# Performance work log

Measured on AMD Instinct MI355X. Metric: run time of the kernel, lower is better.

## Reference

```python
import jax, jax.numpy as jnp
import numpy as np

NUM_HEADS = 16


def setup_inputs() -> dict:
    key = jax.random.key(0)
    ks = jax.random.split(key, 7)
    B, Nq, Nkv = 8, 1024, 2048
    q_dim, kv_dim, hidden = 1024, 1152, 1024
    s = 0.02
    return {
        "vision_latents": jax.random.normal(ks[0], (B, Nkv, kv_dim), jnp.float32),
        "queries": jax.random.normal(ks[1], (B, Nq, q_dim), jnp.float32),
        "attention_mask": jnp.zeros((B, Nkv), dtype=bool),
        "Wq": jax.random.normal(ks[2], (hidden, q_dim), jnp.float32) * s,
        "Wk": jax.random.normal(ks[3], (hidden, kv_dim), jnp.float32) * s,
        "Wv": jax.random.normal(ks[4], (hidden, kv_dim), jnp.float32) * s,
        "Wo": jax.random.normal(ks[5], (hidden, hidden), jnp.float32) * s,
    }


def reference(vision_latents, queries, attention_mask, Wq, Wk, Wv, Wo):
    B, Nq, _ = queries.shape
    Nkv = vision_latents.shape[1]
    H = NUM_HEADS
    hidden = Wq.shape[0]
    D = hidden // H  # head_dim

    # projections (nn.Linear: x @ W.T), split heads -> [B, H, S, D]
    q = (queries @ Wq.T).reshape(B, Nq, H, D).transpose(0, 2, 1, 3)
    k = (vision_latents @ Wk.T).reshape(B, Nkv, H, D).transpose(0, 2, 1, 3)
    v = (vision_latents @ Wv.T).reshape(B, Nkv, H, D).transpose(0, 2, 1, 3)

    scale = 1.0 / np.sqrt(D).astype(np.float32)
    scores = jnp.einsum("bhqd,bhkd->bhqk", q, k) * scale  # [B,H,Nq,Nkv]
    scores = jnp.where(attention_mask[:, None, None, :], jnp.float32(-1e9), scores)
    probs = jax.nn.softmax(scores, axis=-1)
    attn = jnp.einsum("bhqk,bhkd->bhqd", probs, v)  # [B,H,Nq,D]
    attn = attn.transpose(0, 2, 1, 3).reshape(B, Nq, hidden)
    return attn @ Wo.T
```

## Files before the change

kernel.cpp:

```cpp
#include <hip/hip_runtime.h>
#include <stdint.h>

typedef __attribute__((ext_vector_type(8))) __bf16 bf16x8;
typedef __attribute__((ext_vector_type(4))) float f32x4;
typedef __attribute__((ext_vector_type(4))) unsigned short u16x4;
typedef __attribute__((ext_vector_type(4))) unsigned char u8x4;

#define DEV __device__ __forceinline__

DEV unsigned short f2bf(float f) {
  return __builtin_bit_cast(unsigned short, (__bf16)f);
}

DEV void gload16(const void* g, void* l) {
  __builtin_amdgcn_global_load_lds(
      (const __attribute__((address_space(1))) unsigned int*)g,
      (__attribute__((address_space(3))) unsigned int*)l, 16, 0, 0);
}

__global__ __launch_bounds__(256) void cvt_bf16_kernel(
    const float* __restrict__ in, unsigned short* __restrict__ out, int n4) {
  int i = blockIdx.x * blockDim.x + threadIdx.x;
  int stride = gridDim.x * blockDim.x;
  const f32x4* in4 = (const f32x4*)in;
  u16x4* out4 = (u16x4*)out;
  for (; i < n4; i += stride) {
    f32x4 v = in4[i];
    u16x4 o;
    o[0] = f2bf(v[0]); o[1] = f2bf(v[1]); o[2] = f2bf(v[2]); o[3] = f2bf(v[3]);
    out4[i] = o;
  }
}

template <int EPI>
__global__ __launch_bounds__(256, 2) void gemm_bt_kernel(
    const unsigned short* __restrict__ A, const unsigned short* __restrict__ W,
    void* __restrict__ Cout, int M, int N, int K, int logS) {
  __shared__ unsigned short sA[128 * 32];
  __shared__ unsigned short sB[128 * 32];
  const int t = threadIdx.x;
  const int w = t >> 6;
  const int lane = t & 63;
  const int lr = lane & 15;
  const int kg = lane >> 4;
  const int row0 = blockIdx.y * 128;
  const int col0 = blockIdx.x * 128;

  const unsigned short* srcA = A + (size_t)(row0 + (t >> 2)) * K + (t & 3) * 8;
  const unsigned short* srcB = W + (size_t)(col0 + (t >> 2)) * K + (t & 3) * 8;
  const size_t rowSkip = (size_t)64 * K;

  char* sAb = (char*)sA + w * 1024;
  char* sBb = (char*)sB + w * 1024;

  f32x4 acc[4][4];
#pragma unroll
  for (int i = 0; i < 4; i++)
#pragma unroll
    for (int j = 0; j < 4; j++) acc[i][j] = f32x4{0.f, 0.f, 0.f, 0.f};

  const int wr = (w >> 1) * 64;
  const int wc = (w & 1) * 64;

  for (int k0 = 0; k0 < K; k0 += 32) {
    __syncthreads();
    gload16(srcA, sAb);
    gload16(srcA + rowSkip, sAb + 4096);
    gload16(srcB, sBb);
    gload16(srcB + rowSkip, sBb + 4096);
    srcA += 32;
    srcB += 32;
    __syncthreads();

    bf16x8 af[4], bfr[4];
#pragma unroll
    for (int mi = 0; mi < 4; mi++)
      af[mi] = *(const bf16x8*)&sA[(wr + mi * 16 + lr) * 32 + kg * 8];
#pragma unroll
    for (int ni = 0; ni < 4; ni++)
      bfr[ni] = *(const bf16x8*)&sB[(wc + ni * 16 + lr) * 32 + kg * 8];
#pragma unroll
    for (int mi = 0; mi < 4; mi++)
#pragma unroll
      for (int ni = 0; ni < 4; ni++)
        acc[mi][ni] = __builtin_amdgcn_mfma_f32_16x16x32_bf16(
            af[mi], bfr[ni], acc[mi][ni], 0, 0, 0);
  }

  const int S1 = 1 << logS;
  if (EPI == 2) {
    float* O = (float*)Cout;
#pragma unroll
    for (int mi = 0; mi < 4; mi++) {
      int gm0 = row0 + wr + mi * 16 + kg * 4;
#pragma unroll
      for (int ni = 0; ni < 4; ni++) {
        int gn = col0 + wc + ni * 16 + lr;
#pragma unroll
        for (int j = 0; j < 4; j++)
          O[(size_t)(gm0 + j) * N + gn] = acc[mi][ni][j];
      }
    }
  } else if (EPI == 0) {
    unsigned short* O = (unsigned short*)Cout;
#pragma unroll
    for (int mi = 0; mi < 4; mi++) {
      int gm0 = row0 + wr + mi * 16 + kg * 4;
      int b = gm0 >> logS;
      int s = gm0 & (S1 - 1);
#pragma unroll
      for (int ni = 0; ni < 4; ni++) {
        int gn = col0 + wc + ni * 16 + lr;
        int h = gn >> 6, d = gn & 63;
        size_t base = (((size_t)(b * 16 + h) << logS) + s) * 64 + d;
#pragma unroll
        for (int j = 0; j < 4; j++)
          O[base + (size_t)j * 64] = f2bf(acc[mi][ni][j]);
      }
    }
  } else {
    unsigned short* O = (unsigned short*)Cout;
#pragma unroll
    for (int mi = 0; mi < 4; mi++) {
      int gm0 = row0 + wr + mi * 16 + kg * 4;
      int b = gm0 >> logS;
      int s = gm0 & (S1 - 1);
#pragma unroll
      for (int ni = 0; ni < 4; ni++) {
        int gn = col0 + wc + ni * 16 + lr;
        int h = gn >> 6, d = gn & 63;
        u16x4 pk;
#pragma unroll
        for (int j = 0; j < 4; j++) pk[j] = f2bf(acc[mi][ni][j]);
        *(u16x4*)&O[(((size_t)(b * 16 + h) * 64 + d) << logS) + s] = pk;
      }
    }
  }
}

__global__ __launch_bounds__(256, 4) void flash_kernel(
    const unsigned short* __restrict__ Qb, const unsigned short* __restrict__ Kb,
    const unsigned short* __restrict__ Vt, const unsigned char* __restrict__ mask,
    unsigned short* __restrict__ attn) {
  constexpr int NQ = 1024, NKV = 2048, H = 16;
  constexpr float K1 = 0.18033688011112042f;
  __shared__ unsigned short sK[64 * 64];
  __shared__ unsigned short sV[64 * 64];
  __shared__ unsigned short sP[4][32 * 72];

  const int t = threadIdx.x;
  const int w = t >> 6;
  const int lane = t & 63;
  const int c = lane & 15;
  const int g = lane >> 4;
  const int n = blockIdx.x;
  const int bh = n & 127;
  const int b = bh >> 4;
  const int q0 = (n >> 7) * 128 + w * 32;

  bf16x8 qfrag[2][2];
#pragma unroll
  for (int qf = 0; qf < 2; qf++)
#pragma unroll
    for (int kf = 0; kf < 2; kf++)
      qfrag[qf][kf] = *(const bf16x8*)&Qb[((size_t)bh * NQ + q0 + qf * 16 + c) * 64 +
                                          kf * 32 + g * 8];

  const int srow = t >> 3;
  const int sw = (t & 7) ^ (srow & 7);
  const unsigned short* srcK = Kb + ((size_t)bh * NKV + srow) * 64 + sw * 8;
  const unsigned short* srcV = Vt + ((size_t)bh * 64 + srow) * NKV + sw * 8;
  char* sKb = (char*)sK + w * 1024;
  char* sVb = (char*)sV + w * 1024;

  float lrun[2] = {0.f, 0.f};
  f32x4 acc_o[2][4];
#pragma unroll
  for (int i = 0; i < 2; i++)
#pragma unroll
    for (int j = 0; j < 4; j++) acc_o[i][j] = f32x4{0.f, 0.f, 0.f, 0.f};

  const unsigned char* mrow = mask + (size_t)b * NKV;

  for (int kv0 = 0; kv0 < NKV; kv0 += 64) {
    __syncthreads();
    gload16(srcK, sKb);
    gload16(srcK + 32 * 64, sKb + 4096);
    gload16(srcV, sVb);
    gload16(srcV + (size_t)32 * NKV, sVb + 4096);
    srcK += 64 * 64;
    srcV += 64;
    __syncthreads();

    f32x4 accs[4][2];
#pragma unroll
    for (int kvf = 0; kvf < 4; kvf++) {
      int row = kvf * 16 + c;
      const char* rb = (const char*)sK + row * 128;
      bf16x8 ka = *(const bf16x8*)(rb + ((g) ^ (row & 7)) * 16);
      bf16x8 kb = *(const bf16x8*)(rb + ((4 + g) ^ (row & 7)) * 16);
#pragma unroll
      for (int qf = 0; qf < 2; qf++) {
        f32x4 z = f32x4{0.f, 0.f, 0.f, 0.f};
        z = __builtin_amdgcn_mfma_f32_16x16x32_bf16(ka, qfrag[qf][0], z, 0, 0, 0);
        accs[kvf][qf] =
            __builtin_amdgcn_mfma_f32_16x16x32_bf16(kb, qfrag[qf][1], z, 0, 0, 0);
      }
    }

    float mb[4][4];
#pragma unroll
    for (int kvf = 0; kvf < 4; kvf++) {
      u8x4 mm = *(const u8x4*)&mrow[kv0 + kvf * 16 + g * 4];
#pragma unroll
      for (int j = 0; j < 4; j++) mb[kvf][j] = mm[j] ? -30000.0f : 0.0f;
    }

#pragma unroll
    for (int qf = 0; qf < 2; qf++) {
      float ssum = 0.f;
#pragma unroll
      for (int kvf = 0; kvf < 4; kvf++) {
        u16x4 pk;
#pragma unroll
        for (int j = 0; j < 4; j++) {
          float p = exp2f(accs[kvf][qf][j] * K1 + mb[kvf][j]);
          ssum += p;
          pk[j] = f2bf(p);
        }
        *(u16x4*)&sP[w][(qf * 16 + c) * 72 + kvf * 16 + g * 4] = pk;
      }
      ssum += __shfl_xor(ssum, 16);
      ssum += __shfl_xor(ssum, 32);
      lrun[qf] += ssum;
    }

#pragma unroll
    for (int kvs = 0; kvs < 2; kvs++) {
      bf16x8 pa[2];
#pragma unroll
      for (int mi = 0; mi < 2; mi++)
        pa[mi] = *(const bf16x8*)&sP[w][(mi * 16 + c) * 72 + kvs * 32 + g * 8];
#pragma unroll
      for (int nf = 0; nf < 4; nf++) {
        int row = nf * 16 + c;
        bf16x8 vb = *(const bf16x8*)((const char*)sV + row * 128 +
                                     ((kvs * 4 + g) ^ (row & 7)) * 16);
#pragma unroll
        for (int mi = 0; mi < 2; mi++)
          acc_o[mi][nf] = __builtin_amdgcn_mfma_f32_16x16x32_bf16(
              pa[mi], vb, acc_o[mi][nf], 0, 0, 0);
      }
    }
  }

  const int h = bh & 15;
#pragma unroll
  for (int mi = 0; mi < 2; mi++) {
    f32x4 rj;
#pragma unroll
    for (int j = 0; j < 4; j++) rj[j] = 1.0f / __shfl(lrun[mi], g * 4 + j);
    size_t qbase = (size_t)b * NQ + q0 + mi * 16 + g * 4;
#pragma unroll
    for (int j = 0; j < 4; j++) {
      size_t rowb = ((qbase + j) * H + h) * 64;
#pragma unroll
      for (int nf = 0; nf < 4; nf++)
        attn[rowb + nf * 16 + c] = f2bf(acc_o[mi][nf][j] * rj[j]);
    }
  }
}

extern "C" void kernel_launch(void* const* d_in, const int* in_sizes, int n_in,
                              void* d_out, int out_size, void* d_ws, size_t ws_size,
                              hipStream_t stream) {
  const float* vision = (const float*)d_in[0];
  const float* queries = (const float*)d_in[1];
  const unsigned char* mask = (const unsigned char*)d_in[2];
  const float* Wq = (const float*)d_in[3];
  const float* Wk = (const float*)d_in[4];
  const float* Wv = (const float*)d_in[5];
  const float* Wo = (const float*)d_in[6];

  constexpr int B = 8, NQ = 1024, NKV = 2048, HID = 1024, KVD = 1152;
  constexpr size_t nQin = (size_t)B * NQ * HID;
  constexpr size_t nVis = (size_t)B * NKV * KVD;
  constexpr size_t nWq = (size_t)HID * HID;
  constexpr size_t nWk = (size_t)HID * KVD;
  constexpr size_t nQb = (size_t)B * 16 * NQ * 64;
  constexpr size_t nKb = (size_t)B * 16 * NKV * 64;

  constexpr size_t need = (2 * (nWq + nWk) + nVis + nQb + 2 * nKb) * 2;
  if (ws_size < need) {
    hipMemsetAsync(d_out, 0, (size_t)out_size * sizeof(float), stream);
    return;
  }

  char* p = (char*)d_ws;
  unsigned short* wqb = (unsigned short*)p;  p += nWq * 2;
  unsigned short* wkb = (unsigned short*)p;  p += nWk * 2;
  unsigned short* wvb = (unsigned short*)p;  p += nWk * 2;
  unsigned short* wob = (unsigned short*)p;  p += nWq * 2;
  unsigned short* slotA = (unsigned short*)p; p += nVis * 2;
  unsigned short* Qb = (unsigned short*)p;   p += nQb * 2;
  unsigned short* Kbf = (unsigned short*)p;  p += nKb * 2;
  unsigned short* Vtb = (unsigned short*)p;

  unsigned short* qbf = slotA;
  unsigned short* vbf = slotA;
  unsigned short* attnb = slotA;

  auto cvt = [&](const float* in, unsigned short* out, size_t n) {
    int n4 = (int)(n / 4);
    int blocks = (n4 + 255) / 256;
    if (blocks > 2048) blocks = 2048;
    cvt_bf16_kernel<<<dim3(blocks), dim3(256), 0, stream>>>(in, out, n4);
  };
  cvt(Wq, wqb, nWq);
  cvt(Wk, wkb, nWk);
  cvt(Wv, wvb, nWk);
  cvt(Wo, wob, nWq);

  cvt(queries, qbf, nQin);
  gemm_bt_kernel<0><<<dim3(8, 64), dim3(256), 0, stream>>>(qbf, wqb, Qb, 8192, 1024, 1024, 10);

  cvt(vision, vbf, nVis);
  gemm_bt_kernel<0><<<dim3(8, 128), dim3(256), 0, stream>>>(vbf, wkb, Kbf, 16384, 1024, 1152, 11);
  gemm_bt_kernel<1><<<dim3(8, 128), dim3(256), 0, stream>>>(vbf, wvb, Vtb, 16384, 1024, 1152, 11);

  flash_kernel<<<dim3(1024), dim3(256), 0, stream>>>(Qb, Kbf, Vtb, mask, attnb);

  gemm_bt_kernel<2><<<dim3(8, 64), dim3(256), 0, stream>>>(attnb, wob, d_out, 8192, 1024, 1024, 10);
}
```

Baseline: 484.5 us.

## Fuse K/V projections into one GEMM and read K/V from global memory in flash

Merges the K and V projection GEMMs into a single launch with N=2048, which relies on Wk and Wv being contiguous in the workspace and on K and Vt being contiguous. The flash kernel drops its LDS staging of K/V and the block barriers, loading fragments straight from global memory and relying on cache hits. Blocks are remapped so neighbouring blocks share a head, the occupancy hint drops to 3, and raw v_exp/v_rcp instructions replace exp2f and division. The risk is exposed global-load latency and uncoalesced fragment loads where LDS staging used to hide them.

```diff
diff --git a/kernel.cpp b/kernel.cpp
--- a/kernel.cpp
+++ b/kernel.cpp
@@ -10,6 +10,17 @@
 
 DEV unsigned short f2bf(float f) {
   return __builtin_bit_cast(unsigned short, (__bf16)f);
+}
+
+DEV float fast_exp2(float x) {
+  float r;
+  asm("v_exp_f32 %0, %1" : "=v"(r) : "v"(x));
+  return r;
+}
+DEV float fast_rcp(float x) {
+  float r;
+  asm("v_rcp_f32 %0, %1" : "=v"(r) : "v"(x));
+  return r;
 }
 
 DEV void gload16(const void* g, void* l) {
@@ -120,32 +131,40 @@
     }
   } else {
     unsigned short* O = (unsigned short*)Cout;
+    constexpr size_t VOFF = (size_t)8 * 16 * 2048 * 64;
 #pragma unroll
     for (int mi = 0; mi < 4; mi++) {
       int gm0 = row0 + wr + mi * 16 + kg * 4;
-      int b = gm0 >> logS;
-      int s = gm0 & (S1 - 1);
+      int b = gm0 >> 11;
+      int s = gm0 & 2047;
 #pragma unroll
       for (int ni = 0; ni < 4; ni++) {
         int gn = col0 + wc + ni * 16 + lr;
-        int h = gn >> 6, d = gn & 63;
-        u16x4 pk;
-#pragma unroll
-        for (int j = 0; j < 4; j++) pk[j] = f2bf(acc[mi][ni][j]);
-        *(u16x4*)&O[(((size_t)(b * 16 + h) * 64 + d) << logS) + s] = pk;
-      }
-    }
-  }
-}
-
-__global__ __launch_bounds__(256, 4) void flash_kernel(
+        if (gn < 1024) {
+          int h = gn >> 6, d = gn & 63;
+          size_t base = (((size_t)(b * 16 + h) << 11) + s) * 64 + d;
+#pragma unroll
+          for (int j = 0; j < 4; j++)
+            O[base + (size_t)j * 64] = f2bf(acc[mi][ni][j]);
+        } else {
+          int gn2 = gn - 1024;
+          int h = gn2 >> 6, d = gn2 & 63;
+          u16x4 pk;
+#pragma unroll
+          for (int j = 0; j < 4; j++) pk[j] = f2bf(acc[mi][ni][j]);
+          *(u16x4*)&O[VOFF + (((size_t)(b * 16 + h) * 64 + d) << 11) + s] = pk;
+        }
+      }
+    }
+  }
+}
+
+__global__ __launch_bounds__(256, 3) void flash_kernel(
     const unsigned short* __restrict__ Qb, const unsigned short* __restrict__ Kb,
     const unsigned short* __restrict__ Vt, const unsigned char* __restrict__ mask,
     unsigned short* __restrict__ attn) {
   constexpr int NQ = 1024, NKV = 2048, H = 16;
   constexpr float K1 = 0.18033688011112042f;
-  __shared__ unsigned short sK[64 * 64];
-  __shared__ unsigned short sV[64 * 64];
   __shared__ unsigned short sP[4][32 * 72];
 
   const int t = threadIdx.x;
@@ -154,9 +173,9 @@
   const int c = lane & 15;
   const int g = lane >> 4;
   const int n = blockIdx.x;
-  const int bh = n & 127;
+  const int bh = (n & 7) + ((n >> 6) << 3);
   const int b = bh >> 4;
-  const int q0 = (n >> 7) * 128 + w * 32;
+  const int q0 = (((n >> 3) & 7) << 7) + w * 32;
 
   bf16x8 qfrag[2][2];
 #pragma unroll
@@ -166,12 +185,9 @@
       qfrag[qf][kf] = *(const bf16x8*)&Qb[((size_t)bh * NQ + q0 + qf * 16 + c) * 64 +
                                           kf * 32 + g * 8];
 
-  const int srow = t >> 3;
-  const int sw = (t & 7) ^ (srow & 7);
-  const unsigned short* srcK = Kb + ((size_t)bh * NKV + srow) * 64 + sw * 8;
-  const unsigned short* srcV = Vt + ((size_t)bh * 64 + srow) * NKV + sw * 8;
-  char* sKb = (char*)sK + w * 1024;
-  char* sVb = (char*)sV + w * 1024;
+  const unsigned short* Kbase = Kb + (size_t)bh * NKV * 64;
+  const unsigned short* Vbase = Vt + (size_t)bh * 64 * NKV;
+  const unsigned char* mrow = mask + (size_t)b * NKV;
 
   float lrun[2] = {0.f, 0.f};
   f32x4 acc_o[2][4];
@@ -180,33 +196,29 @@
 #pragma unroll
     for (int j = 0; j < 4; j++) acc_o[i][j] = f32x4{0.f, 0.f, 0.f, 0.f};
 
-  const unsigned char* mrow = mask + (size_t)b * NKV;
-
   for (int kv0 = 0; kv0 < NKV; kv0 += 64) {
-    __syncthreads();
-    gload16(srcK, sKb);
-    gload16(srcK + 32 * 64, sKb + 4096);
-    gload16(srcV, sVb);
-    gload16(srcV + (size_t)32 * NKV, sVb + 4096);
-    srcK += 64 * 64;
-    srcV += 64;
-    __syncthreads();
-
     f32x4 accs[4][2];
 #pragma unroll
     for (int kvf = 0; kvf < 4; kvf++) {
-      int row = kvf * 16 + c;
-      const char* rb = (const char*)sK + row * 128;
-      bf16x8 ka = *(const bf16x8*)(rb + ((g) ^ (row & 7)) * 16);
-      bf16x8 kb = *(const bf16x8*)(rb + ((4 + g) ^ (row & 7)) * 16);
+      const unsigned short* kr = Kbase + (size_t)(kv0 + kvf * 16 + c) * 64 + g * 8;
+      bf16x8 ka = *(const bf16x8*)kr;
+      bf16x8 kb2 = *(const bf16x8*)(kr + 32);
 #pragma unroll
       for (int qf = 0; qf < 2; qf++) {
         f32x4 z = f32x4{0.f, 0.f, 0.f, 0.f};
         z = __builtin_amdgcn_mfma_f32_16x16x32_bf16(ka, qfrag[qf][0], z, 0, 0, 0);
         accs[kvf][qf] =
-            __builtin_amdgcn_mfma_f32_16x16x32_bf16(kb, qfrag[qf][1], z, 0, 0, 0);
-      }
-    }
+            __builtin_amdgcn_mfma_f32_16x16x32_bf16(kb2, qfrag[qf][1], z, 0, 0, 0);
+      }
+    }
+
+    bf16x8 vb[4][2];
+#pragma unroll
+    for (int nf = 0; nf < 4; nf++)
+#pragma unroll
+      for (int kvs = 0; kvs < 2; kvs++)
+        vb[nf][kvs] = *(const bf16x8*)(Vbase + (size_t)(nf * 16 + c) * NKV + kv0 +
+                                       kvs * 32 + g * 8);
 
     float mb[4][4];
 #pragma unroll
@@ -224,7 +236,7 @@
         u16x4 pk;
 #pragma unroll
         for (int j = 0; j < 4; j++) {
-          float p = exp2f(accs[kvf][qf][j] * K1 + mb[kvf][j]);
+          float p = fast_exp2(accs[kvf][qf][j] * K1 + mb[kvf][j]);
           ssum += p;
           pk[j] = f2bf(p);
         }
@@ -242,15 +254,11 @@
       for (int mi = 0; mi < 2; mi++)
         pa[mi] = *(const bf16x8*)&sP[w][(mi * 16 + c) * 72 + kvs * 32 + g * 8];
 #pragma unroll
-      for (int nf = 0; nf < 4; nf++) {
-        int row = nf * 16 + c;
-        bf16x8 vb = *(const bf16x8*)((const char*)sV + row * 128 +
-                                     ((kvs * 4 + g) ^ (row & 7)) * 16);
+      for (int nf = 0; nf < 4; nf++)
 #pragma unroll
         for (int mi = 0; mi < 2; mi++)
           acc_o[mi][nf] = __builtin_amdgcn_mfma_f32_16x16x32_bf16(
-              pa[mi], vb, acc_o[mi][nf], 0, 0, 0);
-      }
+              pa[mi], vb[nf][kvs], acc_o[mi][nf], 0, 0, 0);
     }
   }
 
@@ -259,7 +267,7 @@
   for (int mi = 0; mi < 2; mi++) {
     f32x4 rj;
 #pragma unroll
-    for (int j = 0; j < 4; j++) rj[j] = 1.0f / __shfl(lrun[mi], g * 4 + j);
+    for (int j = 0; j < 4; j++) rj[j] = fast_rcp(__shfl(lrun[mi], g * 4 + j));
     size_t qbase = (size_t)b * NQ + q0 + mi * 16 + g * 4;
 #pragma unroll
     for (int j = 0; j < 4; j++) {
@@ -309,6 +317,7 @@
   unsigned short* qbf = slotA;
   unsigned short* vbf = slotA;
   unsigned short* attnb = slotA;
+  (void)wvb; (void)Vtb;
 
   auto cvt = [&](const float* in, unsigned short* out, size_t n) {
     int n4 = (int)(n / 4);
@@ -325,8 +334,7 @@
   gemm_bt_kernel<0><<<dim3(8, 64), dim3(256), 0, stream>>>(qbf, wqb, Qb, 8192, 1024, 1024, 10);
 
   cvt(vision, vbf, nVis);
-  gemm_bt_kernel<0><<<dim3(8, 128), dim3(256), 0, stream>>>(vbf, wkb, Kbf, 16384, 1024, 1152, 11);
-  gemm_bt_kernel<1><<<dim3(8, 128), dim3(256), 0, stream>>>(vbf, wvb, Vtb, 16384, 1024, 1152, 11);
+  gemm_bt_kernel<3><<<dim3(16, 128), dim3(256), 0, stream>>>(vbf, wkb, Kbf, 16384, 2048, 1152, 11);
 
   flash_kernel<<<dim3(1024), dim3(256), 0, stream>>>(Qb, Kbf, Vtb, mask, attnb);
 
```

After: 598.5 us. +23.5%, slower.

## Fuse K and V projections into one GEMM, remap flash blocks, use fast exp/rcp

Applied to the files above, without the earlier changes.

Runs the K and V projections as one GEMM with N=2048, relying on Wk and Wv (and the K and V outputs) sitting next to each other in the workspace. An epilogue branch writes the K half row-major and the V half transposed at a fixed offset. The flash kernel's block-to-(batch-head, query-tile) mapping is reordered so neighbouring blocks share a batch-head, which should improve K/V cache reuse. The softmax exp2 and the final reciprocal now use raw v_exp_f32/v_rcp_f32, trading a little accuracy and denormal handling for fewer instructions.

```diff
diff --git a/kernel.cpp b/kernel.cpp
--- a/kernel.cpp
+++ b/kernel.cpp
@@ -10,6 +10,17 @@
 
 DEV unsigned short f2bf(float f) {
   return __builtin_bit_cast(unsigned short, (__bf16)f);
+}
+
+DEV float fast_exp2(float x) {
+  float r;
+  asm("v_exp_f32 %0, %1" : "=v"(r) : "v"(x));
+  return r;
+}
+DEV float fast_rcp(float x) {
+  float r;
+  asm("v_rcp_f32 %0, %1" : "=v"(r) : "v"(x));
+  return r;
 }
 
 DEV void gload16(const void* g, void* l) {
@@ -120,19 +131,29 @@
     }
   } else {
     unsigned short* O = (unsigned short*)Cout;
+    constexpr size_t VOFF = (size_t)8 * 16 * 2048 * 64;
 #pragma unroll
     for (int mi = 0; mi < 4; mi++) {
       int gm0 = row0 + wr + mi * 16 + kg * 4;
-      int b = gm0 >> logS;
-      int s = gm0 & (S1 - 1);
+      int b = gm0 >> 11;
+      int s = gm0 & 2047;
 #pragma unroll
       for (int ni = 0; ni < 4; ni++) {
         int gn = col0 + wc + ni * 16 + lr;
-        int h = gn >> 6, d = gn & 63;
-        u16x4 pk;
-#pragma unroll
-        for (int j = 0; j < 4; j++) pk[j] = f2bf(acc[mi][ni][j]);
-        *(u16x4*)&O[(((size_t)(b * 16 + h) * 64 + d) << logS) + s] = pk;
+        if (gn < 1024) {
+          int h = gn >> 6, d = gn & 63;
+          size_t base = (((size_t)(b * 16 + h) << 11) + s) * 64 + d;
+#pragma unroll
+          for (int j = 0; j < 4; j++)
+            O[base + (size_t)j * 64] = f2bf(acc[mi][ni][j]);
+        } else {
+          int gn2 = gn - 1024;
+          int h = gn2 >> 6, d = gn2 & 63;
+          u16x4 pk;
+#pragma unroll
+          for (int j = 0; j < 4; j++) pk[j] = f2bf(acc[mi][ni][j]);
+          *(u16x4*)&O[VOFF + (((size_t)(b * 16 + h) * 64 + d) << 11) + s] = pk;
+        }
       }
     }
   }
@@ -154,9 +175,9 @@
   const int c = lane & 15;
   const int g = lane >> 4;
   const int n = blockIdx.x;
-  const int bh = n & 127;
+  const int bh = (n & 7) + ((n >> 6) << 3);
   const int b = bh >> 4;
-  const int q0 = (n >> 7) * 128 + w * 32;
+  const int q0 = (((n >> 3) & 7) << 7) + w * 32;
 
   bf16x8 qfrag[2][2];
 #pragma unroll
@@ -224,7 +245,7 @@
         u16x4 pk;
 #pragma unroll
         for (int j = 0; j < 4; j++) {
-          float p = exp2f(accs[kvf][qf][j] * K1 + mb[kvf][j]);
+          float p = fast_exp2(accs[kvf][qf][j] * K1 + mb[kvf][j]);
           ssum += p;
           pk[j] = f2bf(p);
         }
@@ -259,7 +280,7 @@
   for (int mi = 0; mi < 2; mi++) {
     f32x4 rj;
 #pragma unroll
-    for (int j = 0; j < 4; j++) rj[j] = 1.0f / __shfl(lrun[mi], g * 4 + j);
+    for (int j = 0; j < 4; j++) rj[j] = fast_rcp(__shfl(lrun[mi], g * 4 + j));
     size_t qbase = (size_t)b * NQ + q0 + mi * 16 + g * 4;
 #pragma unroll
     for (int j = 0; j < 4; j++) {
@@ -309,6 +330,7 @@
   unsigned short* qbf = slotA;
   unsigned short* vbf = slotA;
   unsigned short* attnb = slotA;
+  (void)wvb; (void)Vtb;
 
   auto cvt = [&](const float* in, unsigned short* out, size_t n) {
     int n4 = (int)(n / 4);
@@ -325,8 +347,7 @@
   gemm_bt_kernel<0><<<dim3(8, 64), dim3(256), 0, stream>>>(qbf, wqb, Qb, 8192, 1024, 1024, 10);
 
   cvt(vision, vbf, nVis);
-  gemm_bt_kernel<0><<<dim3(8, 128), dim3(256), 0, stream>>>(vbf, wkb, Kbf, 16384, 1024, 1152, 11);
-  gemm_bt_kernel<1><<<dim3(8, 128), dim3(256), 0, stream>>>(vbf, wvb, Vtb, 16384, 1024, 1152, 11);
+  gemm_bt_kernel<3><<<dim3(16, 128), dim3(256), 0, stream>>>(vbf, wkb, Kbf, 16384, 2048, 1152, 11);
 
   flash_kernel<<<dim3(1024), dim3(256), 0, stream>>>(Qb, Kbf, Vtb, mask, attnb);
 
```

New measurement: 424.7 us. 1.14x faster.
